# Kernel optimization log

Hardware: AMD Instinct MI355X
Metric: run time of the kernel (lower is better)

## Reference

```python
import jax, jax.numpy as jnp
import numpy as np

EPS = 1e-6


def setup_inputs() -> dict:
    key = jax.random.key(0)
    k1, _ = jax.random.split(key)
    L, D = 128, 262144
    slots = jax.random.normal(k1, (L, D), dtype=jnp.float32)
    temperature = jnp.ones((), dtype=jnp.float32)  # temperature = 1.0
    return {"slots": slots, "temperature": temperature, "length": L}


def reference(slots, temperature, length):
    # slots: [L, D]; pairwise cosine similarity (torch: x.y / max(|x||y|, eps))
    L = length
    norms = jnp.sqrt(jnp.sum(slots * slots, axis=1))                # [L]
    gram = jnp.einsum('id,jd->ij', slots, slots)                    # [L, L]
    sim = gram / jnp.maximum(norms[:, None] * norms[None, :], EPS)  # [L, L]
    logits = sim / temperature
    E = jnp.exp(logits)                                             # [L, L]
    # denominator for pair (i, j): sum_{k != j} exp(sim(i,k)/T)  (k=i included)
    denom = jnp.sum(E, axis=1, keepdims=True) - E                   # [L, L]
    log_ratio = logits - jnp.log(denom)                             # log(num/den)
    idx = jnp.arange(L)
    penalty = jnp.abs(idx[:, None] - idx[None, :]).astype(slots.dtype)  # |i-j|
    upper = (idx[:, None] < idx[None, :]).astype(slots.dtype)           # i < j
    total = jnp.sum(-log_ratio * penalty * upper)
    # original divides by i*j/2 with final loop values i=j=length-1
    total = total / ((L - 1) * (L - 1) / 2.0)
    return total
```

## Files before the change

kernel.cpp:

```cpp
#include <hip/hip_runtime.h>
#include <hip/hip_bf16.h>

typedef __attribute__((ext_vector_type(8))) short bf16x8;
typedef __attribute__((ext_vector_type(4))) float f32x4;

constexpr int L     = 128;
constexpr int BK    = 256;
constexpr int GRID  = 256;
constexpr int PITCH = BK * 2;

__device__ inline float blo(unsigned w) { unsigned v = w << 16;          return __builtin_bit_cast(float, v); }
__device__ inline float bhi(unsigned w) { unsigned v = w & 0xffff0000u;  return __builtin_bit_cast(float, v); }

__global__ __launch_bounds__(512, 2)
void gram_kernel(const float* __restrict__ slots, uint2* __restrict__ p16,
                 unsigned* __restrict__ cnt, int D, int nChunks, int G) {
    __shared__ __align__(16) char lds[2][L * PITCH];
    const int t    = threadIdx.x;
    const int wave = t >> 6;
    const int lane = t & 63;

    if (blockIdx.x == 0 && t == 0) *cnt = 0;

    f32x4 acc[8];
#pragma unroll
    for (int c = 0; c < 8; ++c) acc[c] = (f32x4)0.f;

    float4 ld[16];

    auto issue = [&](int chunk) {
#pragma unroll
        for (int q = 0; q < 16; ++q) {
            const int row = wave * 16 + q;
            ld[q] = *reinterpret_cast<const float4*>(
                slots + (size_t)row * D + (size_t)chunk * BK + lane * 4);
        }
    };
    auto commit = [&](int buf) {
#pragma unroll
        for (int q = 0; q < 16; ++q) {
            const int row = wave * 16 + q;
            const unsigned* f = reinterpret_cast<const unsigned*>(&ld[q]);
            uint2 w;
            w.x = __builtin_amdgcn_perm(f[1], f[0], 0x07060302u);
            w.y = __builtin_amdgcn_perm(f[3], f[2], 0x07060302u);
            int byte = (lane * 8) ^ ((row & 7) << 4);
            *reinterpret_cast<uint2*>(&lds[buf][row * PITCH + byte]) = w;
        }
    };
    auto ldfrag = [&](int buf, int row, int kk) -> bf16x8 {
        int byte = row * PITCH + ((kk * 2 + ((lane >> 4) << 4)) ^ ((row & 7) << 4));
        return *reinterpret_cast<const bf16x8*>(&lds[buf][byte]);
    };

    issue(blockIdx.x);
    commit(0);
    __syncthreads();

    int k = 0;
    for (int c = blockIdx.x; c < nChunks; c += G, ++k) {
        const int cur = k & 1;
        const bool more = (c + G < nChunks);
        if (more) issue(c + G);

#pragma unroll
        for (int kk = 0; kk < BK; kk += 32) {
            bf16x8 a = ldfrag(cur, wave * 16 + (lane & 15), kk);
#pragma unroll
            for (int cc = 0; cc < 8; ++cc) {
                bf16x8 b = ldfrag(cur, cc * 16 + (lane & 15), kk);
                acc[cc] = __builtin_amdgcn_mfma_f32_16x16x32_bf16(a, b, acc[cc], 0, 0, 0);
            }
        }

        if (more) commit(cur ^ 1);
        __syncthreads();
    }

    uint2* pb = p16 + (size_t)blockIdx.x * 4096;
#pragma unroll
    for (int cc = 0; cc < 8; ++cc) {
        const unsigned* a = reinterpret_cast<const unsigned*>(&acc[cc]);
        uint2 w;
        w.x = __builtin_amdgcn_perm(a[1], a[0], 0x07060302u);
        w.y = __builtin_amdgcn_perm(a[3], a[2], 0x07060302u);
        pb[cc * 512 + t] = w;
    }
}

__global__ __launch_bounds__(256)
void reduce_finalize(const uint2* __restrict__ p16, float* __restrict__ gram,
                     unsigned* __restrict__ cnt,
                     const float* __restrict__ temperature, float* __restrict__ out,
                     int G) {
    __shared__ __align__(16) float g[L * L];
    __shared__ float norms[L];
    __shared__ float wred[4];
    __shared__ unsigned ticket_s;
    const int t   = threadIdx.x;
    const int sl  = t & 15;
    const int sub = t >> 4;
    const int j   = blockIdx.x * 16 + sl;

    f32x4 s = (f32x4)0.f;
#pragma unroll 8
    for (int b = sub; b < G; b += 16) {
        const uint2 u = p16[(size_t)b * 4096 + j];
        s[0] += blo(u.x); s[1] += bhi(u.x);
        s[2] += blo(u.y); s[3] += bhi(u.y);
    }
    f32x4* red = reinterpret_cast<f32x4*>(g);
    red[sub * 16 + sl] = s;
    __syncthreads();
    if (t < 16) {
        f32x4 s4 = red[t];
#pragma unroll
        for (int w = 1; w < 16; ++w) s4 += red[w * 16 + t];
        const int myj  = blockIdx.x * 16 + t;
        const int cc   = myj >> 9;
        const int tenc = myj & 511;
        const int wv = tenc >> 6, ln = tenc & 63;
        const int growb = wv * 16 + ((ln >> 4) << 2);
        const int gcol  = cc * 16 + (ln & 15);
#pragma unroll
        for (int q = 0; q < 4; ++q) gram[(growb + q) * L + gcol] = s4[q];
    }

    __syncthreads();
    if (t == 0) {
        __threadfence();
        ticket_s = atomicAdd(cnt, 1u);
    }
    __syncthreads();
    if (ticket_s != (unsigned)(gridDim.x - 1)) return;
    __threadfence();

#pragma unroll
    for (int q = 0; q < 16; ++q) {
        int i = t + 256 * q;
        *reinterpret_cast<float4*>(&g[i * 4]) =
            *reinterpret_cast<const float4*>(&gram[i * 4]);
    }
    __syncthreads();
    if (t < L) norms[t] = sqrtf(g[t * L + t]);
    __syncthreads();

    const float invT = 1.0f / temperature[0];
    const int r = t >> 1;
    const int q = t & 1;
    const float ni = norms[r];

    float ps = 0.f;
    for (int jj = q; jj < L; jj += 2) {
        float sim = g[r * L + jj] / fmaxf(ni * norms[jj], 1e-6f);
        ps += __expf(sim * invT);
    }
    ps += __shfl_xor(ps, 1);
    const float rowsum = ps;

    float tot = 0.f;
    for (int jj = q; jj < L; jj += 2) {
        if (jj > r) {
            float logit = (g[r * L + jj] / fmaxf(ni * norms[jj], 1e-6f)) * invT;
            tot += -(logit - __logf(rowsum - __expf(logit))) * (float)(jj - r);
        }
    }
#pragma unroll
    for (int m = 1; m < 64; m <<= 1) tot += __shfl_xor(tot, m);
    if ((t & 63) == 0) wred[t >> 6] = tot;
    __syncthreads();
    if (t == 0)
        out[0] = (wred[0] + wred[1] + wred[2] + wred[3]) /
                 ((float)(L - 1) * (float)(L - 1) * 0.5f);
}

extern "C" void kernel_launch(void* const* d_in, const int* in_sizes, int n_in,
                              void* d_out, int out_size, void* d_ws, size_t ws_size,
                              hipStream_t stream) {
    const float* slots       = (const float*)d_in[0];
    const float* temperature = (const float*)d_in[1];
    float* out  = (float*)d_out;

    const int D = in_sizes[0] / L;
    const int nChunks = D / BK;
    int G = GRID;
    if (G > nChunks) G = nChunks;

    uint2*    p16  = (uint2*)d_ws;
    float*    gram = (float*)((char*)d_ws + (size_t)G * 32768);
    unsigned* cnt  = (unsigned*)((char*)gram + (size_t)L * L * 4);

    gram_kernel<<<G, 512, 0, stream>>>(slots, p16, cnt, D, nChunks, G);
    reduce_finalize<<<256, 256, 0, stream>>>(p16, gram, cnt, temperature, out, G);
}
```

Before: 56.06 us.

## Pre-pack slots to swizzled bf16 tiles and stage via direct global-to-LDS loads

Adds a separate pack kernel that converts the fp32 slots to bf16 and writes them in the swizzled per-chunk tile layout the GEMM expects. The gram kernel then copies each tile straight into LDS with global_load_lds, dropping the register round-trip and the in-loop conversion. This is meant to cut register pressure and VALU work in the main loop. The cost is an extra pass that reads 128 MB of fp32 and writes 64 MB of bf16 plus a kernel launch, and the GEMM then reads the 64 MB back.

```diff
diff --git a/kernel.cpp b/kernel.cpp
--- a/kernel.cpp
+++ b/kernel.cpp
@@ -12,9 +12,29 @@
 __device__ inline float blo(unsigned w) { unsigned v = w << 16;          return __builtin_bit_cast(float, v); }
 __device__ inline float bhi(unsigned w) { unsigned v = w & 0xffff0000u;  return __builtin_bit_cast(float, v); }
 
+__global__ __launch_bounds__(256)
+void pack_kernel(const float* __restrict__ slots, char* __restrict__ packed, int D) {
+    const size_t total  = (size_t)L * (D >> 2);
+    const size_t stride = (size_t)gridDim.x * 256;
+    for (size_t i = (size_t)blockIdx.x * 256 + threadIdx.x; i < total; i += stride) {
+        const float4 v = reinterpret_cast<const float4*>(slots)[i];
+        const int row   = (int)(i >> 16);
+        const int wf4   = (int)(i & 65535);
+        const int chunk = wf4 >> 6;
+        const int m     = wf4 & 63;
+        const unsigned* f = reinterpret_cast<const unsigned*>(&v);
+        uint2 w;
+        w.x = __builtin_amdgcn_perm(f[1], f[0], 0x07060302u);
+        w.y = __builtin_amdgcn_perm(f[3], f[2], 0x07060302u);
+        const size_t seg  = (size_t)chunk * L + row;
+        const int    byte = (m * 8) ^ ((row & 7) << 4);
+        *reinterpret_cast<uint2*>(packed + seg * PITCH + byte) = w;
+    }
+}
+
 __global__ __launch_bounds__(512, 2)
-void gram_kernel(const float* __restrict__ slots, uint2* __restrict__ p16,
-                 unsigned* __restrict__ cnt, int D, int nChunks, int G) {
+void gram_kernel(const char* __restrict__ packed, uint2* __restrict__ p16,
+                 unsigned* __restrict__ cnt, int nChunks, int G) {
     __shared__ __align__(16) char lds[2][L * PITCH];
     const int t    = threadIdx.x;
     const int wave = t >> 6;
@@ -26,26 +46,15 @@
 #pragma unroll
     for (int c = 0; c < 8; ++c) acc[c] = (f32x4)0.f;
 
-    float4 ld[16];
-
-    auto issue = [&](int chunk) {
-#pragma unroll
-        for (int q = 0; q < 16; ++q) {
-            const int row = wave * 16 + q;
-            ld[q] = *reinterpret_cast<const float4*>(
-                slots + (size_t)row * D + (size_t)chunk * BK + lane * 4);
-        }
-    };
-    auto commit = [&](int buf) {
-#pragma unroll
-        for (int q = 0; q < 16; ++q) {
-            const int row = wave * 16 + q;
-            const unsigned* f = reinterpret_cast<const unsigned*>(&ld[q]);
-            uint2 w;
-            w.x = __builtin_amdgcn_perm(f[1], f[0], 0x07060302u);
-            w.y = __builtin_amdgcn_perm(f[3], f[2], 0x07060302u);
-            int byte = (lane * 8) ^ ((row & 7) << 4);
-            *reinterpret_cast<uint2*>(&lds[buf][row * PITCH + byte]) = w;
+    auto stage = [&](int buf, int tile) {
+        const char* src = packed + (size_t)tile * (L * PITCH);
+#pragma unroll
+        for (int q = 0; q < 8; ++q) {
+            const int off = (wave * 8 + q) * 1024;
+            __builtin_amdgcn_global_load_lds(
+                (const __attribute__((address_space(1))) unsigned*)(src + off + lane * 16),
+                (__attribute__((address_space(3))) unsigned*)&lds[buf][off],
+                16, 0, 0);
         }
     };
     auto ldfrag = [&](int buf, int row, int kk) -> bf16x8 {
@@ -53,15 +62,14 @@
         return *reinterpret_cast<const bf16x8*>(&lds[buf][byte]);
     };
 
-    issue(blockIdx.x);
-    commit(0);
+    stage(0, blockIdx.x);
     __syncthreads();
 
     int k = 0;
     for (int c = blockIdx.x; c < nChunks; c += G, ++k) {
         const int cur = k & 1;
         const bool more = (c + G < nChunks);
-        if (more) issue(c + G);
+        if (more) stage(cur ^ 1, c + G);
 
 #pragma unroll
         for (int kk = 0; kk < BK; kk += 32) {
@@ -72,8 +80,6 @@
                 acc[cc] = __builtin_amdgcn_mfma_f32_16x16x32_bf16(a, b, acc[cc], 0, 0, 0);
             }
         }
-
-        if (more) commit(cur ^ 1);
         __syncthreads();
     }
 
@@ -186,10 +192,12 @@
     int G = GRID;
     if (G > nChunks) G = nChunks;
 
-    uint2*    p16  = (uint2*)d_ws;
-    float*    gram = (float*)((char*)d_ws + (size_t)G * 32768);
-    unsigned* cnt  = (unsigned*)((char*)gram + (size_t)L * L * 4);
-
-    gram_kernel<<<G, 512, 0, stream>>>(slots, p16, cnt, D, nChunks, G);
+    char*     packed = (char*)d_ws;
+    uint2*    p16    = (uint2*)(packed + (size_t)nChunks * L * PITCH);
+    float*    gram   = (float*)((char*)p16 + (size_t)G * 32768);
+    unsigned* cnt    = (unsigned*)((char*)gram + (size_t)L * L * 4);
+
+    pack_kernel<<<4096, 256, 0, stream>>>(slots, packed, D);
+    gram_kernel<<<G, 512, 0, stream>>>(packed, p16, cnt, nChunks, G);
     reduce_finalize<<<256, 256, 0, stream>>>(p16, gram, cnt, temperature, out, G);
 }
```

Result: slower. 77.64 us (+38.5%).

## Stage half the rows via direct global-to-LDS loads, halve K chunk

Applied to the files above, without the earlier changes.

Splits each chunk into two halves. Rows 0-63 are loaded straight into LDS as fp32 using global_load_lds with an XOR swizzle and converted to bf16 when fragments are read. Rows 64-127 keep the register path that converts to bf16 before writing LDS. The chunk width drops from 256 to 128 so the mixed-precision buffers fit in LDS. The aim is to cut register pressure and VGPR round trips for staging. In exchange it adds perm work on every fragment read for the fp32 half, doubles LDS reads for that half, and doubles the number of loop iterations and barriers.

```diff
diff --git a/kernel.cpp b/kernel.cpp
--- a/kernel.cpp
+++ b/kernel.cpp
@@ -4,10 +4,13 @@
 typedef __attribute__((ext_vector_type(8))) short bf16x8;
 typedef __attribute__((ext_vector_type(4))) float f32x4;
 
-constexpr int L     = 128;
-constexpr int BK    = 256;
-constexpr int GRID  = 256;
-constexpr int PITCH = BK * 2;
+constexpr int L    = 128;
+constexpr int BK   = 128;
+constexpr int GRID = 256;
+
+constexpr int A_BYTES = 64 * BK * 4;
+constexpr int B_BYTES = 64 * BK * 2;
+constexpr int BUF_BYTES = A_BYTES + B_BYTES;
 
 __device__ inline float blo(unsigned w) { unsigned v = w << 16;          return __builtin_bit_cast(float, v); }
 __device__ inline float bhi(unsigned w) { unsigned v = w & 0xffff0000u;  return __builtin_bit_cast(float, v); }
@@ -15,7 +18,7 @@
 __global__ __launch_bounds__(512, 2)
 void gram_kernel(const float* __restrict__ slots, uint2* __restrict__ p16,
                  unsigned* __restrict__ cnt, int D, int nChunks, int G) {
-    __shared__ __align__(16) char lds[2][L * PITCH];
+    __shared__ __align__(16) char lds[2][BUF_BYTES];
     const int t    = threadIdx.x;
     const int wave = t >> 6;
     const int lane = t & 63;
@@ -26,54 +29,91 @@
 #pragma unroll
     for (int c = 0; c < 8; ++c) acc[c] = (f32x4)0.f;
 
-    float4 ld[16];
-
-    auto issue = [&](int chunk) {
-#pragma unroll
-        for (int q = 0; q < 16; ++q) {
-            const int row = wave * 16 + q;
+    float4 ld[4];
+
+    auto stageA = [&](int buf, int chunk) {
+#pragma unroll
+        for (int q = 0; q < 4; ++q) {
+            const int r0  = wave * 8 + q * 2;
+            const int row = r0 + (lane >> 5);
+            const int u   = (lane & 31) ^ (row & 15);
+            const float* src = slots + (size_t)row * D + (size_t)chunk * BK + u * 4;
+            __builtin_amdgcn_global_load_lds(
+                (const __attribute__((address_space(1))) unsigned*)src,
+                (__attribute__((address_space(3))) unsigned*)&lds[buf][r0 * 512],
+                16, 0, 0);
+        }
+    };
+    auto issueB = [&](int chunk) {
+#pragma unroll
+        for (int q = 0; q < 4; ++q) {
+            int idx  = t + 512 * q;
+            int row  = 64 + (idx >> 5);
+            int col4 = idx & 31;
             ld[q] = *reinterpret_cast<const float4*>(
-                slots + (size_t)row * D + (size_t)chunk * BK + lane * 4);
-        }
-    };
-    auto commit = [&](int buf) {
-#pragma unroll
-        for (int q = 0; q < 16; ++q) {
-            const int row = wave * 16 + q;
+                slots + (size_t)row * D + (size_t)chunk * BK + col4 * 4);
+        }
+    };
+    auto commitB = [&](int buf) {
+#pragma unroll
+        for (int q = 0; q < 4; ++q) {
+            int idx  = t + 512 * q;
+            int rb   = idx >> 5;
+            int col4 = idx & 31;
             const unsigned* f = reinterpret_cast<const unsigned*>(&ld[q]);
             uint2 w;
             w.x = __builtin_amdgcn_perm(f[1], f[0], 0x07060302u);
             w.y = __builtin_amdgcn_perm(f[3], f[2], 0x07060302u);
-            int byte = (lane * 8) ^ ((row & 7) << 4);
-            *reinterpret_cast<uint2*>(&lds[buf][row * PITCH + byte]) = w;
-        }
-    };
-    auto ldfrag = [&](int buf, int row, int kk) -> bf16x8 {
-        int byte = row * PITCH + ((kk * 2 + ((lane >> 4) << 4)) ^ ((row & 7) << 4));
+            int byte = (col4 * 8) ^ ((rb & 7) << 4);
+            *reinterpret_cast<uint2*>(&lds[buf][A_BYTES + rb * 256 + byte]) = w;
+        }
+    };
+    auto ldfragA = [&](int buf, int row, int kk) -> bf16x8 {
+        const int u0 = (kk >> 2) + ((lane >> 4) << 1);
+        const int p0 = u0 ^ (row & 15);
+        const int p1 = (u0 + 1) ^ (row & 15);
+        const char* base = &lds[buf][row * 512];
+        const f32x4 f0 = *reinterpret_cast<const f32x4*>(base + p0 * 16);
+        const f32x4 f1 = *reinterpret_cast<const f32x4*>(base + p1 * 16);
+        const unsigned* a = reinterpret_cast<const unsigned*>(&f0);
+        const unsigned* b = reinterpret_cast<const unsigned*>(&f1);
+        union { bf16x8 v; unsigned w[4]; } r;
+        r.w[0] = __builtin_amdgcn_perm(a[1], a[0], 0x07060302u);
+        r.w[1] = __builtin_amdgcn_perm(a[3], a[2], 0x07060302u);
+        r.w[2] = __builtin_amdgcn_perm(b[1], b[0], 0x07060302u);
+        r.w[3] = __builtin_amdgcn_perm(b[3], b[2], 0x07060302u);
+        return r.v;
+    };
+    auto ldfragB = [&](int buf, int row, int kk) -> bf16x8 {
+        const int rb = row - 64;
+        int byte = A_BYTES + rb * 256 + ((kk * 2 + ((lane >> 4) << 4)) ^ ((rb & 7) << 4));
         return *reinterpret_cast<const bf16x8*>(&lds[buf][byte]);
     };
 
-    issue(blockIdx.x);
-    commit(0);
+    stageA(0, blockIdx.x);
+    issueB(blockIdx.x);
+    commitB(0);
     __syncthreads();
 
     int k = 0;
     for (int c = blockIdx.x; c < nChunks; c += G, ++k) {
         const int cur = k & 1;
         const bool more = (c + G < nChunks);
-        if (more) issue(c + G);
-
+        if (more) { stageA(cur ^ 1, c + G); issueB(c + G); }
+
+        const int rowa = wave * 16 + (lane & 15);
 #pragma unroll
         for (int kk = 0; kk < BK; kk += 32) {
-            bf16x8 a = ldfrag(cur, wave * 16 + (lane & 15), kk);
+            bf16x8 a = (wave < 4) ? ldfragA(cur, rowa, kk) : ldfragB(cur, rowa, kk);
 #pragma unroll
             for (int cc = 0; cc < 8; ++cc) {
-                bf16x8 b = ldfrag(cur, cc * 16 + (lane & 15), kk);
+                const int rowb = cc * 16 + (lane & 15);
+                bf16x8 b = (cc < 4) ? ldfragA(cur, rowb, kk) : ldfragB(cur, rowb, kk);
                 acc[cc] = __builtin_amdgcn_mfma_f32_16x16x32_bf16(a, b, acc[cc], 0, 0, 0);
             }
         }
 
-        if (more) commit(cur ^ 1);
+        if (more) commitB(cur ^ 1);
         __syncthreads();
     }
 
```

New measurement: 57.82 us. +3.1%, slower.
